# Performance work log

Hardware: AMD Instinct MI355X
Metric: run time of the kernel (lower is better)

## Reference

```python
import jax, jax.numpy as jnp
import numpy as np

B = 1024          # sub (= obj) batch size
NUME = 20000      # num entities
NUMR = 8          # num relations
NET = 2 * NUMR + 1  # hetero edge types: r, -r, self
DIMT = 28         # time encoding dim
DIME = 100        # entity embedding dim
DIM = 200         # emb module output dim
H = 4             # history length
HEADS = 4         # GAT heads
OH = DIM // HEADS # GAT per-head out dim
N0 = 160000       # layer-0 src nodes
N1 = 40000        # layer-0 dst / layer-1 src nodes
R = 2 * B * H     # unique roots = layer-1 dst nodes
E0 = 60000        # edges per etype, layer 0
E1 = 16000        # edges per etype, layer 1
K = 500000        # copy mask entries
DIMR = 100        # relation embedding dim
HATT = 4          # self-attention heads
OA = DIM // HATT  # per-head q/k/v dim (Attention out_dim//h)
DIN0 = DIME + DIMT
DIN1 = DIM + DIMT


def setup_inputs() -> dict:
    key = jax.random.key(0)
    ks = jax.random.split(key, 48)
    ri = jax.random.randint
    nrm = lambda i, shp, s=0.05: jax.random.normal(ks[i], shp, jnp.float32) * s
    d = {}
    d['sub'] = ri(ks[0], (B,), 0, NUME)
    d['obj'] = ri(ks[1], (B,), 0, NUME)
    d['rel'] = ri(ks[2], (B,), 0, NUMR)
    d['ts'] = 1000
    d['nid0'] = ri(ks[3], (N0,), 0, NUME * 1000)
    d['root_idx'] = ri(ks[4], (2 * B * H,), 0, R)
    d['src0'] = ri(ks[5], (NET, E0), 0, N0)
    d['dst0'] = ri(ks[6], (NET, E0), 0, N1)
    d['src1'] = ri(ks[7], (NET, E1), 0, N1)
    d['dst1'] = ri(ks[8], (NET, E1), 0, R)
    d['copy_rows'] = ri(ks[9], (K,), 0, 2 * B)
    d['copy_cols'] = ri(ks[10], (K,), 0, NUME)
    # parameters
    d['emb_table'] = nrm(11, (NUME, DIME))
    d['time_freq'] = jnp.asarray(1.0 / 10 ** np.linspace(0, 9, DIMT), jnp.float32)
    d['time_phase'] = jnp.zeros((DIMT,), jnp.float32)
    d['Wg0'] = nrm(12, (NET, DIN0, HEADS, OH))
    d['al0'] = nrm(13, (NET, HEADS, OH))
    d['ar0'] = nrm(14, (NET, HEADS, OH))
    d['bg0'] = jnp.zeros((NET, DIM), jnp.float32)
    d['Wg1'] = nrm(15, (NET, DIN1, HEADS, OH))
    d['al1'] = nrm(16, (NET, HEADS, OH))
    d['ar1'] = nrm(17, (NET, HEADS, OH))
    d['bg1'] = jnp.zeros((NET, DIM), jnp.float32)
    d['ln0_w'] = jnp.ones((H * DIM,), jnp.float32)
    d['ln0_b'] = jnp.zeros((H * DIM,), jnp.float32)
    d['Wq'] = nrm(18, (HATT, DIM, OA))
    d['bq'] = jnp.zeros((HATT, OA), jnp.float32)
    d['Wv'] = nrm(19, (HATT, DIM, OA))
    d['bv'] = jnp.zeros((HATT, OA), jnp.float32)
    d['ln1_w'] = jnp.ones((H * DIM,), jnp.float32)
    d['ln1_b'] = jnp.zeros((H * DIM,), jnp.float32)
    d['Wd1'] = nrm(20, (H * DIM, DIM))
    d['bd1'] = jnp.zeros((DIM,), jnp.float32)
    d['srel_emb'] = nrm(21, (NUMR, DIMR))
    d['orel_emb'] = nrm(22, (NUMR, DIMR))
    d['Wsub'] = nrm(23, (DIM + DIMR, NUME))
    d['bsub'] = jnp.zeros((NUME,), jnp.float32)
    d['Wobj'] = nrm(24, (DIM + DIMR, NUME))
    d['bobj'] = jnp.zeros((NUME,), jnp.float32)
    d['csrel_emb'] = nrm(25, (NUMR, DIMR))
    d['corel_emb'] = nrm(26, (NUMR, DIMR))
    d['cWsub'] = nrm(27, (DIM + DIMR, NUME))
    d['cbsub'] = jnp.zeros((NUME,), jnp.float32)
    d['cWobj'] = nrm(28, (DIM + DIMR, NUME))
    d['cbobj'] = jnp.zeros((NUME,), jnp.float32)
    return d


def _temb(nid, ts, tf, tp):
    t = (ts - nid // NUME).astype(jnp.float32)
    return jnp.cos(t[:, None] * tf + tp)


def _gat(x, Wg, al, ar, bg, src, dst, nd):
    # heterogeneous GATConv over NET relation types, mean-aggregated (DGL HeteroGraphConv)
    msg = jnp.zeros((nd, HEADS, OH), x.dtype)
    for r in range(NET):
        s, d = src[r], dst[r]
        fs = jnp.einsum('ei,iho->eho', x[s], Wg[r])                     # [E,h,o] src feats per edge
        er_n = (jnp.einsum('ni,iho->nho', x[:nd], Wg[r]) * ar[r]).sum(-1)  # [nd,h]
        el = (fs * al[r]).sum(-1)                                       # [E,h]
        e = jax.nn.leaky_relu(el + er_n[d], 0.2)
        m = jax.ops.segment_max(e, d, num_segments=nd)
        a = jnp.exp(e - m[d])
        z = jax.ops.segment_sum(a, d, num_segments=nd)
        alpha = a / z[d]
        msg = msg + jax.ops.segment_sum(alpha[:, :, None] * fs, d, num_segments=nd)
    return jax.nn.relu((msg.reshape(nd, HEADS * OH) + bg.sum(0)) / NET)


def _ln(x, w, b):
    mu = x.mean(-1, keepdims=True)
    v = ((x - mu) ** 2).mean(-1, keepdims=True)
    return (x - mu) / jnp.sqrt(v + 1e-5) * w + b


def reference(sub, obj, rel, ts, nid0, root_idx, src0, dst0, src1, dst1, copy_rows, copy_cols, emb_table, time_freq, time_phase, Wg0, al0, ar0, bg0, Wg1, al1, ar1, bg1, ln0_w, ln0_b, Wq, bq, Wv, bv, ln1_w, ln1_b, Wd1, bd1, srel_emb, orel_emb, Wsub, bsub, Wobj, bobj, csrel_emb, corel_emb, cWsub, cbsub, cWobj, cbobj):
    # --- EmbModule: entity emb + time enc + 2-layer hetero GAT over sampled blocks ---
    h = emb_table[nid0 % NUME]                                   # [N0, DIME]
    x = jnp.concatenate([h, _temb(nid0, ts, time_freq, time_phase)], 1)
    h = _gat(x, Wg0, al0, ar0, bg0, src0, dst0, N1)              # [N1, DIM]
    x = jnp.concatenate([h, _temb(nid0[:N1], ts, time_freq, time_phase)], 1)
    h = _gat(x, Wg1, al1, ar1, bg1, src1, dst1, R)               # [R, DIM]
    hid = h[root_idx].reshape(2 * B, H * DIM)                    # [2B, H*DIM]
    # --- Copy mechanism (on detached last-history embedding) ---
    ch = jax.lax.stop_gradient(hid[:, -DIM:])
    raw_sub = jnp.concatenate([ch[B:], corel_emb[rel]], 1) @ cWsub + cbsub
    raw_obj = jnp.concatenate([ch[:B], csrel_emb[rel]], 1) @ cWobj + cbobj
    raw = jnp.concatenate([raw_sub, raw_obj], 0)                 # [2B, NUME]
    masked = jnp.full((2 * B, NUME), -100.0, raw.dtype).at[copy_rows, copy_cols].set(raw[copy_rows, copy_cols])
    csub, cobj = masked[:B], masked[B:]
    # --- Gen layers: LN -> SelfAttention -> LN -> dense ---
    x = _ln(hid, ln0_w, ln0_b)
    xs = x.reshape(2 * B, H, DIM)
    q = jnp.einsum('bse,heo->bhso', xs, Wq) + bq[:, None, :]     # k == q (w_q reused in source)
    att = jax.nn.softmax(jnp.einsum('bhso,bhto->bhst', q, q), axis=2)  # torch softmax(dim=1)
    v = jnp.einsum('bse,heo->bhso', xs, Wv) + bv[:, None, :]
    ans = jnp.einsum('bhst,bhto->bhso', att, v)                  # [2B,h,S,OA]
    x = jax.nn.relu(ans.transpose(0, 2, 1, 3).reshape(2 * B, H * DIM))
    x = _ln(x, ln1_w, ln1_b)
    x = jax.nn.relu(x @ Wd1 + bd1)                               # [2B, DIM]
    sub_emb, obj_emb = x[:B], x[B:]
    sub_pred = jnp.concatenate([obj_emb, orel_emb[rel]], 1) @ Wsub + bsub
    obj_pred = jnp.concatenate([sub_emb, srel_emb[rel]], 1) @ Wobj + bobj
    return (sub_pred, obj_pred, csub, cobj)
```

## Files before the change

kernel.cpp:

```cpp
#include <hip/hip_runtime.h>
#include <hip/hip_bf16.h>
#include <math.h>

typedef __hip_bfloat16 bf16;
typedef __attribute__((ext_vector_type(8))) short short8;
typedef __attribute__((ext_vector_type(4))) float f32x4;

#define BQ 1024
#define NUME 20000
#define NET 17
#define DIMT 28
#define DIME 100
#define DIM 200
#define HEADS 4
#define OH 50
#define N0 160000
#define N1 40000
#define RNODES 8192
#define E0 60000
#define E1 16000
#define KK 500000
#define DIMR 100
#define HATT 4
#define OA 50
#define DIN0 128
#define DIN1 228
#define HD 800
#define NROWS 2048
#define PKS 10
#define PNT 1250
#define TABW 136

__device__ __forceinline__ float b2f(bf16 v){ return __bfloat162float(v); }
__device__ __forceinline__ bf16 f2b(float v){ return __float2bfloat16(v); }
__device__ __forceinline__ float bs2f(unsigned short u){ return __uint_as_float((unsigned)u << 16); }
__device__ __forceinline__ unsigned short f2bu(float v){ bf16 t = f2b(v); return *reinterpret_cast<unsigned short*>(&t); }

static constexpr int CVT_NREG = 29;
static constexpr int CVT_N[CVT_NREG] = {
  2000000, 28, 28, 435200, 3400, 3400, 3400, 775200, 3400, 3400, 3400,
  800, 800, 40000, 200, 40000, 200, 800, 800, 160000, 200, 800, 800,
  20000, 20000, 800, 800, 20000, 20000
};
static constexpr int CVT_DIN[CVT_NREG] = {
  12,13,14,15,16,17,18,19,20,21,22,23,24,25,26,27,28,29,30,31,32,33,34,36,38,39,40,42,44
};
struct CvtSrcs { const void* p[CVT_NREG]; };
struct CvtMeta { int cum[CVT_NREG+1]; int bcum[CVT_NREG+1]; };

__global__ __launch_bounds__(64) void k_detect(const unsigned* tfw, unsigned* flag){
  if (threadIdx.x == 0) flag[0] = ((tfw[0] & 0xFFFFu) == 0u) ? 1u : 0u;
}

__global__ __launch_bounds__(256) void k_cvt(CvtSrcs srcs, CvtMeta meta, bf16* dst, const unsigned* flagp){
  int b = blockIdx.x;
  int r = 0;
  while (meta.bcum[r+1] <= b) r++;
  int i = (b - meta.bcum[r])*256 + threadIdx.x;
  int n = meta.cum[r+1] - meta.cum[r];
  if (i >= n) return;
  bool f32m = flagp[0] != 0u;
  bf16 v;
  if (f32m) v = f2b(((const float*)srcs.p[r])[i]);
  else      v = ((const bf16*)srcs.p[r])[i];
  dst[meta.cum[r] + i] = v;
}

__global__ __launch_bounds__(256) void k_fill_u32(unsigned* p, unsigned v, long n){
  long i = (long)blockIdx.x*256 + threadIdx.x;
  if (i < n) p[i] = v;
}

__global__ __launch_bounds__(256) void k_fill_out(void* outb, const unsigned* flagp){
  bool f32m = flagp[0] != 0u;
  long nwords = f32m ? (long)2*BQ*NUME : (long)BQ*NUME;
  long i = (long)blockIdx.x*256 + threadIdx.x;
  if (i >= nwords) return;
  unsigned* p = (unsigned*)((char*)outb + (size_t)2*BQ*NUME * (f32m ? 4 : 2));
  p[i] = f32m ? 0xC2C80000u : 0xC2C8C2C8u;
}

__global__ __launch_bounds__(256) void k_prep_w(const bf16* Wg, const bf16* al, const bf16* ar,
                                                float* wal, float* war, int DIN){
  int idx = blockIdx.x*256 + threadIdx.x;
  int total = NET*DIN*4;
  if (idx >= total) return;
  int h = idx & 3; int ri = idx >> 2; int i = ri % DIN; int r = ri / DIN;
  const bf16* wrow = Wg + ((size_t)(r*DIN + i))*HEADS*OH + h*OH;
  const bf16* alr = al + (size_t)(r*HEADS + h)*OH;
  const bf16* arr = ar + (size_t)(r*HEADS + h)*OH;
  float sl=0.f, sr=0.f;
  for (int o=0;o<OH;o++){ float w=b2f(wrow[o]); sl += w*b2f(alr[o]); sr += w*b2f(arr[o]); }
  wal[idx]=sl; war[idx]=sr;
}

__global__ __launch_bounds__(256) void k_pack(const bf16* Wg, bf16* wpk, int DIN, int KS){
  int idx = blockIdx.x*256 + threadIdx.x;
  int total = NET*KS*13*512;
  if (idx >= total) return;
  int j = idx & 7, lane = (idx>>3) & 63;
  int rem = idx >> 9;
  int nt = rem % 13, rks = rem / 13;
  int ks = rks % KS, r = rks / KS;
  int k = ks*32 + (lane>>4)*8 + j;
  int n = nt*16 + (lane&15);
  bf16 v = f2b(0.f);
  if (k < DIN && n < 200) v = Wg[((size_t)r*DIN + k)*200 + n];
  wpk[idx] = v;
}

__global__ __launch_bounds__(256) void k_pack_walr(const float* wal, const float* war, bf16* wpkE,
                                                   int DIN, int KS){
  int idx = blockIdx.x*256 + threadIdx.x;
  int total = KS*9*512;
  if (idx >= total) return;
  int j = idx & 7, lane = (idx>>3) & 63;
  int rem = idx >> 9;
  int nt = rem % 9, ks = rem / 9;
  int k = ks*32 + (lane>>4)*8 + j;
  int c = nt*16 + (lane&15);
  float v = 0.f;
  if (k < DIN && c < TABW){
    int r = c >> 3, q = c & 7;
    const float* wsrc = (q < 4) ? wal : war;
    v = wsrc[((size_t)r*DIN + k)*4 + (q & 3)];
  }
  wpkE[idx] = f2b(v);
}

template<int DIN, int KS>
__global__ __launch_bounds__(256) void k_elr(const bf16* __restrict__ x, const bf16* __restrict__ wpkE,
                                             float* __restrict__ tab){
  constexpr int KM = KS*32;
  constexpr int SR = KM + 8;
  __shared__ bf16 xs[64*SR];
  int rb = blockIdx.x*64;
  int t = threadIdx.x;
  constexpr int CH = KM/4;
  for (int c = t; c < 64*CH; c += 256){
    int m = c / CH, j4 = c % CH;
    uint2 v = make_uint2(0u,0u);
    if (j4*4 < DIN) v = *(const uint2*)(x + (size_t)(rb+m)*DIN + j4*4);
    *(uint2*)(xs + m*SR + j4*4) = v;
  }
  __syncthreads();
  int lane = t & 63, w = t >> 6;
  int n_idx = lane & 15, quad = lane >> 4;
  const short8* wp8 = (const short8*)wpkE;
  for (int mt=0; mt<4; mt++){
    short8 a[KS];
    const bf16* ab = xs + (size_t)(mt*16 + n_idx)*SR + quad*8;
    #pragma unroll
    for (int ks=0; ks<KS; ks++) a[ks] = *(const short8*)(ab + ks*32);
    int m = rb + mt*16 + n_idx;
    for (int nt=w; nt<9; nt+=4){
      const short8* bp = wp8 + (size_t)nt*64 + lane;
      f32x4 acc = {0.f,0.f,0.f,0.f};
      #pragma unroll
      for (int ks=0; ks<KS; ks++){
        short8 b = bp[(size_t)ks*9*64];
        acc = __builtin_amdgcn_mfma_f32_16x16x32_bf16(b, a[ks], acc, 0, 0, 0);
      }
      int nbase = nt*16 + quad*4;
      if (nbase < TABW){
        float4 o; o.x=acc[0]; o.y=acc[1]; o.z=acc[2]; o.w=acc[3];
        *(float4*)(tab + (size_t)m*TABW + nbase) = o;
      }
    }
  }
}

__global__ __launch_bounds__(256) void k_edge_lite(const float* __restrict__ tab,
                                                   const int* __restrict__ src, const int* __restrict__ dst,
                                                   bf16* abuf, float* z, int nE, int nd){
  int idx = blockIdx.x*256 + threadIdx.x;
  if (idx >= NET*nE) return;
  int r = idx / nE;
  int s = src[idx], d = dst[idx];
  float4 el = *(const float4*)(tab + (size_t)s*TABW + r*8);
  float4 er = *(const float4*)(tab + (size_t)d*TABW + r*8 + 4);
  float ev[4] = {el.x+er.x, el.y+er.y, el.z+er.z, el.w+er.w};
  float* zp = z + ((size_t)r*nd + d)*4;
  bf16* ao = abuf + (size_t)idx*4;
  #pragma unroll
  for (int h=0;h<4;h++){
    float v = ev[h];
    v = v>0.f ? v : 0.2f*v;
    float a = expf(fminf(v, 80.f));
    ao[h] = f2b(a);
    atomicAdd(&zp[h], a);
  }
}

template<int DIN>
__global__ __launch_bounds__(256) void k_er(const bf16* __restrict__ x, const float* __restrict__ war,
                                            bf16* __restrict__ er, int nd){
  int idx = blockIdx.x*256 + threadIdx.x;
  if (idx >= NET*nd) return;
  int r = idx / nd, n = idx % nd;
  const ushort4* xr = (const ushort4*)(x + (size_t)n*DIN);
  const float4* w = (const float4*)(war + (size_t)r*DIN*4);
  float a0=0.f,a1=0.f,a2=0.f,a3=0.f;
  #pragma unroll 4
  for (int i=0;i<DIN/4;i++){
    ushort4 xv = xr[i];
    float x0=bs2f(xv.x), x1=bs2f(xv.y), x2=bs2f(xv.z), x3=bs2f(xv.w);
    float4 w0=w[4*i], w1=w[4*i+1], w2=w[4*i+2], w3=w[4*i+3];
    a0 += x0*w0.x + x1*w1.x + x2*w2.x + x3*w3.x;
    a1 += x0*w0.y + x1*w1.y + x2*w2.y + x3*w3.y;
    a2 += x0*w0.z + x1*w1.z + x2*w2.z + x3*w3.z;
    a3 += x0*w0.w + x1*w1.w + x2*w2.w + x3*w3.w;
  }
  bf16* e = er + (size_t)idx*4;
  e[0]=f2b(a0); e[1]=f2b(a1); e[2]=f2b(a2); e[3]=f2b(a3);
}

template<int DIN>
__global__ __launch_bounds__(256) void k_edge(const bf16* __restrict__ x, const float* __restrict__ wal,
                                              const bf16* __restrict__ er,
                                              const int* __restrict__ src, const int* __restrict__ dst,
                                              bf16* abuf, float* z, int nE, int nd){
  int idx = blockIdx.x*256 + threadIdx.x;
  if (idx >= NET*nE) return;
  int r = idx / nE;
  int s = src[idx], d = dst[idx];
  const ushort4* xr = (const ushort4*)(x + (size_t)s*DIN);
  const float4* w = (const float4*)(wal + (size_t)r*DIN*4);
  float a0=0.f,a1=0.f,a2=0.f,a3=0.f;
  #pragma unroll 4
  for (int i=0;i<DIN/4;i++){
    ushort4 xv = xr[i];
    float x0=bs2f(xv.x), x1=bs2f(xv.y), x2=bs2f(xv.z), x3=bs2f(xv.w);
    float4 w0=w[4*i], w1=w[4*i+1], w2=w[4*i+2], w3=w[4*i+3];
    a0 += x0*w0.x + x1*w1.x + x2*w2.x + x3*w3.x;
    a1 += x0*w0.y + x1*w1.y + x2*w2.y + x3*w3.y;
    a2 += x0*w0.z + x1*w1.z + x2*w2.z + x3*w3.z;
    a3 += x0*w0.w + x1*w1.w + x2*w2.w + x3*w3.w;
  }
  float acc[4] = {a0,a1,a2,a3};
  const bf16* ern = er + ((size_t)r*nd + d)*4;
  float* zp = z + ((size_t)r*nd + d)*4;
  bf16* ao = abuf + (size_t)idx*4;
  #pragma unroll
  for (int h=0;h<4;h++){
    float v = acc[h] + b2f(ern[h]);
    v = v>0.f ? v : 0.2f*v;
    float a = expf(fminf(v, 80.f));
    ao[h] = f2b(a);
    atomicAdd(&zp[h], a);
  }
}

__global__ __launch_bounds__(256) void k_count(const int* __restrict__ dst, long n, unsigned* cnt){
  long i = (long)blockIdx.x*256 + threadIdx.x;
  if (i >= n) return;
  atomicAdd(&cnt[dst[i]], 1u);
}

__global__ __launch_bounds__(256) void k_scan(const unsigned* __restrict__ cnt, unsigned* offs, unsigned* cur, int n){
  __shared__ unsigned part[256];
  __shared__ unsigned tot;
  int t = threadIdx.x;
  int chunk = (n + 255)/256;
  int lo = t*chunk, hi = lo+chunk; if (hi > n) hi = n; if (lo > n) lo = n;
  unsigned s = 0;
  for (int i=lo;i<hi;i++) s += cnt[i];
  part[t] = s;
  __syncthreads();
  if (t==0){
    unsigned r = 0;
    for (int i=0;i<256;i++){ unsigned v = part[i]; part[i] = r; r += v; }
    tot = r;
  }
  __syncthreads();
  unsigned run = part[t];
  for (int i=lo;i<hi;i++){ offs[i]=run; cur[i]=run; run += cnt[i]; }
  if (t==0) offs[n] = tot;
}

__global__ __launch_bounds__(256) void k_fillcsr(const int* __restrict__ dst, long n, unsigned* cur, int* posar){
  long i = (long)blockIdx.x*256 + threadIdx.x;
  if (i >= n) return;
  unsigned pos = atomicAdd(&cur[dst[i]], 1u);
  posar[i] = (int)pos;
}

template<int DIN, int KS>
__global__ __launch_bounds__(256) void k_acc_mfma(const bf16* __restrict__ x, const bf16* __restrict__ wpk,
                                                  const bf16* __restrict__ abuf, const float* __restrict__ z,
                                                  const int* __restrict__ src, const int* __restrict__ dst,
                                                  const int* __restrict__ posar,
                                                  float* msg, bf16* fbuf, int nE, int nd, int r0, int mode){
  constexpr int KM = KS*32;
  constexpr int SR = KM + 8;
  __shared__ bf16 xs[64*SR];
  __shared__ float alpha_s[64*4];
  __shared__ int sdst[64], ssrc[64], spos[64];
  int r = r0 + blockIdx.y;
  int eb = blockIdx.x*64;
  int me = min(64, nE - eb);
  int t = threadIdx.x;
  if (t < 64){
    int v_src=0, v_dst=0, v_pos=0;
    if (t < me){
      v_src = src[(size_t)r*nE + eb + t];
      v_dst = dst[(size_t)r*nE + eb + t];
      if (posar) v_pos = posar[(size_t)(r - r0)*nE + eb + t];
    }
    ssrc[t]=v_src; sdst[t]=v_dst; spos[t]=v_pos;
  }
  __syncthreads();
  {
    int m = t>>2, h = t&3;
    float al = 0.f;
    if (m < me){
      float a = b2f(abuf[((size_t)r*nE + eb + m)*4 + h]);
      float zz = z[((size_t)r*nd + sdst[m])*4 + h];
      al = a / fmaxf(zz, 1e-30f);
    }
    alpha_s[m*4+h] = al;
  }
  constexpr int CH = KM/4;
  for (int c = t; c < 64*CH; c += 256){
    int m = c / CH, j4 = c % CH;
    uint2 v = make_uint2(0u,0u);
    if (m < me && j4*4 < DIN) v = *(const uint2*)(x + (size_t)ssrc[m]*DIN + j4*4);
    *(uint2*)(xs + m*SR + j4*4) = v;
  }
  __syncthreads();

  int lane = t & 63, w = t >> 6;
  int n_idx = lane & 15, quad = lane >> 4;
  const short8* wpk8 = (const short8*)wpk;
  for (int mt=0; mt<4; mt++){
    short8 a[KS];
    const bf16* abase = xs + (size_t)(mt*16 + n_idx)*SR + quad*8;
    #pragma unroll
    for (int ks=0; ks<KS; ks++) a[ks] = *(const short8*)(abase + ks*32);
    int m = mt*16 + n_idx;
    for (int nt=w; nt<13; nt+=4){
      const short8* bp = wpk8 + (((size_t)r*KS)*13 + nt)*64 + lane;
      f32x4 acc = {0.f,0.f,0.f,0.f};
      #pragma unroll
      for (int ks=0; ks<KS; ks++){
        short8 b = bp[(size_t)ks*13*64];
        acc = __builtin_amdgcn_mfma_f32_16x16x32_bf16(b, a[ks], acc, 0, 0, 0);
      }
      int nbase = nt*16 + quad*4;
      if (nbase < 200 && m < me){
        if (mode == 0){
          #pragma unroll
          for (int reg=0; reg<4; reg++){
            int n = nbase + reg;
            atomicAdd(&msg[(size_t)sdst[m]*200 + n], acc[reg] * alpha_s[m*4 + n/50]);
          }
        } else {
          ushort4 pk;
          { int n=nbase;   pk.x = f2bu(acc[0] * alpha_s[m*4 + n/50]); }
          { int n=nbase+1; pk.y = f2bu(acc[1] * alpha_s[m*4 + n/50]); }
          { int n=nbase+2; pk.z = f2bu(acc[2] * alpha_s[m*4 + n/50]); }
          { int n=nbase+3; pk.w = f2bu(acc[3] * alpha_s[m*4 + n/50]); }
          *(ushort4*)(fbuf + (size_t)spos[m]*200 + nbase) = pk;
        }
      }
    }
  }
}

__global__ __launch_bounds__(256) void k_gather_seq(const bf16* __restrict__ F, const unsigned* __restrict__ offs,
                                                    float* __restrict__ msg, int nd, int accum){
  int w = threadIdx.x >> 6, lane = threadIdx.x & 63;
  int d = blockIdx.x*4 + w;
  if (d >= nd) return;
  unsigned k0 = offs[d], k1 = offs[d+1];
  if (lane < 50){
    float a0=0.f, a1=0.f, a2=0.f, a3=0.f;
    for (unsigned k=k0; k<k1; k++){
      ushort4 v = *(const ushort4*)(F + (size_t)k*200 + lane*4);
      a0 += bs2f(v.x); a1 += bs2f(v.y); a2 += bs2f(v.z); a3 += bs2f(v.w);
    }
    float4* out = (float4*)(msg + (size_t)d*200 + lane*4);
    if (accum){ float4 p = *out; a0 += p.x; a1 += p.y; a2 += p.z; a3 += p.w; }
    float4 o; o.x=a0; o.y=a1; o.z=a2; o.w=a3;
    *out = o;
  }
}

__global__ __launch_bounds__(256) void k_bgs(const bf16* bg0, const bf16* bg1, float* bgs0, float* bgs1){
  int j = blockIdx.x*256 + threadIdx.x;
  if (j < DIM){ float s=0.f; for(int r=0;r<NET;r++) s += b2f(bg0[r*DIM+j]); bgs0[j]=s; }
  else if (j < 2*DIM){ int jj=j-DIM; float s=0.f; for(int r=0;r<NET;r++) s += b2f(bg1[r*DIM+jj]); bgs1[jj]=s; }
}

__global__ __launch_bounds__(256) void k_build_x0(const int* nid0, const int* ts_p, const bf16* emb,
                                                  const bf16* tf, const bf16* tp, bf16* x0){
  long idx = (long)blockIdx.x*256 + threadIdx.x;
  if (idx >= (long)N0*DIN0) return;
  int n = idx / DIN0, j = idx % DIN0;
  int nid = nid0[n];
  bf16 v;
  if (j < DIME) v = emb[(size_t)(nid % NUME)*DIME + j];
  else {
    float t = (float)(ts_p[0] - nid / NUME);
    int jj = j - DIME;
    v = f2b(cosf(t * b2f(tf[jj]) + b2f(tp[jj])));
  }
  x0[idx] = v;
}

__global__ __launch_bounds__(256) void k_build_x1(const int* nid0, const int* ts_p, const float* msg0,
                                                  const float* bgs0, const bf16* tf, const bf16* tp, bf16* x1){
  long idx = (long)blockIdx.x*256 + threadIdx.x;
  if (idx >= (long)N1*DIN1) return;
  int n = idx / DIN1, j = idx % DIN1;
  bf16 v;
  if (j < DIM){
    v = f2b(fmaxf((msg0[(size_t)n*DIM + j] + bgs0[j]) * (1.0f/NET), 0.0f));
  } else {
    int nid = nid0[n];
    float t = (float)(ts_p[0] - nid / NUME);
    int jj = j - DIM;
    v = f2b(cosf(t * b2f(tf[jj]) + b2f(tp[jj])));
  }
  x1[idx] = v;
}

__global__ __launch_bounds__(256) void k_hid(const float* msg1, const float* bgs1, const int* root_idx, float* hid){
  long idx = (long)blockIdx.x*256 + threadIdx.x;
  if (idx >= (long)NROWS*HD) return;
  int b = idx / HD, c = idx % HD;
  int s = c / DIM, j = c % DIM;
  int n = root_idx[b*4 + s];
  hid[idx] = fmaxf((msg1[(size_t)n*DIM + j] + bgs1[j]) * (1.0f/NET), 0.0f);
}

__global__ __launch_bounds__(256) void k_att_ln(const float* __restrict__ hid,
                                                const bf16* ln0w, const bf16* ln0b,
                                                const bf16* Wq, const bf16* bq,
                                                const bf16* Wv, const bf16* bv,
                                                const bf16* ln1w, const bf16* ln1b,
                                                float* __restrict__ x3){
  __shared__ float xs[HD], qs[HD], vs[HD], att_s[64], red[16];
  __shared__ float mu_s, rs_s;
  int b = blockIdx.x, t = threadIdx.x;
  int lane = t & 63, wid = t >> 6;
  const float* xr = hid + (size_t)b*HD;
  float s=0.f, s2=0.f;
  for (int j=t;j<HD;j+=256){ float v=xr[j]; s+=v; s2+=v*v; }
  for (int off=32; off; off>>=1){ s += __shfl_down(s,off); s2 += __shfl_down(s2,off); }
  if (lane==0){ red[wid]=s; red[8+wid]=s2; }
  __syncthreads();
  if (t==0){
    float S = red[0]+red[1]+red[2]+red[3];
    float S2 = red[8]+red[9]+red[10]+red[11];
    float mu = S * (1.0f/HD);
    float var = fmaxf(S2 * (1.0f/HD) - mu*mu, 0.f);
    mu_s = mu; rs_s = rsqrtf(var + 1e-5f);
  }
  __syncthreads();
  { float mu=mu_s, rs=rs_s;
    for (int j=t;j<HD;j+=256) xs[j] = (xr[j]-mu)*rs*b2f(ln0w[j]) + b2f(ln0b[j]); }
  __syncthreads();
  for (int idx=t; idx<HD; idx+=256){
    int ha = idx/200, srow=(idx%200)/50, o=idx%50;
    const float* xrow = xs + srow*200;
    const bf16* wq = Wq + (size_t)ha*DIM*OA + o;
    const bf16* wv = Wv + (size_t)ha*DIM*OA + o;
    float q=0.f, v=0.f;
    for (int e=0;e<DIM;e++){ float xv=xrow[e]; q += xv*b2f(wq[(size_t)e*OA]); v += xv*b2f(wv[(size_t)e*OA]); }
    qs[idx] = q + b2f(bq[ha*OA+o]);
    vs[idx] = v + b2f(bv[ha*OA+o]);
  }
  __syncthreads();
  if (t < 64){
    int ha=t>>4, srow=(t>>2)&3, tt=t&3;
    const float* qa = qs + ha*200 + srow*50;
    const float* qb = qs + ha*200 + tt*50;
    float sc=0.f;
    for (int o=0;o<50;o++) sc += qa[o]*qb[o];
    att_s[ha*16 + srow*4 + tt] = sc;
  }
  __syncthreads();
  if (t < 16){
    int ha=t>>2, tt=t&3;
    float m=-1e30f;
    for (int srow=0;srow<4;srow++) m = fmaxf(m, att_s[ha*16+srow*4+tt]);
    float ex[4]; float zz=0.f;
    for (int srow=0;srow<4;srow++){ ex[srow]=expf(att_s[ha*16+srow*4+tt]-m); zz+=ex[srow]; }
    for (int srow=0;srow<4;srow++) att_s[ha*16+srow*4+tt] = ex[srow]/zz;
  }
  __syncthreads();
  for (int idx=t; idx<HD; idx+=256){
    int ha = idx/200, srow=(idx%200)/50, o=idx%50;
    float a=0.f;
    for (int tt=0;tt<4;tt++) a += att_s[ha*16+srow*4+tt]*vs[ha*200+tt*50+o];
    xs[srow*200 + ha*50 + o] = fmaxf(a, 0.f);
  }
  __syncthreads();
  s=0.f; s2=0.f;
  for (int j=t;j<HD;j+=256){ float v=xs[j]; s+=v; s2+=v*v; }
  for (int off=32; off; off>>=1){ s += __shfl_down(s,off); s2 += __shfl_down(s2,off); }
  if (lane==0){ red[wid]=s; red[8+wid]=s2; }
  __syncthreads();
  if (t==0){
    float S = red[0]+red[1]+red[2]+red[3];
    float S2 = red[8]+red[9]+red[10]+red[11];
    float mu = S * (1.0f/HD);
    float var = fmaxf(S2 * (1.0f/HD) - mu*mu, 0.f);
    mu_s = mu; rs_s = rsqrtf(var + 1e-5f);
  }
  __syncthreads();
  { float mu=mu_s, rs=rs_s;
    for (int j=t;j<HD;j+=256) x3[(size_t)b*HD + j] = (xs[j]-mu)*rs*b2f(ln1w[j]) + b2f(ln1b[j]); }
}

__global__ __launch_bounds__(256) void k_d1(const float* x3, const bf16* Wd1, const bf16* bd1, float* x4){
  __shared__ float xs[8*HD];
  int rb = blockIdx.x*8, t = threadIdx.x;
  for (int idx=t; idx<8*HD; idx+=256) xs[idx] = x3[(size_t)rb*HD + idx];
  __syncthreads();
  if (t < DIM){
    float acc[8] = {0,0,0,0,0,0,0,0};
    for (int k=0;k<HD;k++){
      float w = b2f(Wd1[(size_t)k*DIM + t]);
      #pragma unroll
      for (int r=0;r<8;r++) acc[r] += xs[r*HD+k]*w;
    }
    float bb = b2f(bd1[t]);
    for (int r=0;r<8;r++) x4[(size_t)(rb+r)*DIM + t] = fmaxf(acc[r]+bb, 0.f);
  }
}

__global__ __launch_bounds__(256) void k_pack_pred(const void* Wsub, const void* Wobj, bf16* wpkP,
                                                    const unsigned* flagp){
  long idx = (long)blockIdx.x*256 + threadIdx.x;
  long total = (long)2*PKS*PNT*512;
  if (idx >= total) return;
// ... 95 lines not shown
  int rb = blockIdx.y*16;
  int cb = blockIdx.x*512;
  int t = threadIdx.x;
  for (int idx=t; idx<16*300; idx+=256){
    int r = idx/300, i = idx%300;
    int row = rb + r;
    float v = (i < DIM) ? xemb[(size_t)row*DIM + i]
                        : b2f(relemb[(size_t)rel[row]*DIMR + (i-DIM)]);
    As[r*304+i] = v;
  }
  __syncthreads();
  int c0 = cb + t, c1 = cb + 256 + t;
  bool g0 = c0 < NUME, g1 = c1 < NUME;
  float acc0[16], acc1[16];
  #pragma unroll
  for (int r=0;r<16;r++){ acc0[r]=0.f; acc1[r]=0.f; }
  if (f32m){
    const float* W32 = (const float*)W;
    for (int k=0;k<300;k++){
      float w0 = g0 ? W32[(size_t)k*NUME + c0] : 0.f;
      float w1 = g1 ? W32[(size_t)k*NUME + c1] : 0.f;
      #pragma unroll
      for (int r=0;r<16;r++){ float a = As[r*304+k]; acc0[r] += a*w0; acc1[r] += a*w1; }
    }
  } else {
    const bf16* W16 = (const bf16*)W;
    for (int k=0;k<300;k++){
      float w0 = g0 ? b2f(W16[(size_t)k*NUME + c0]) : 0.f;
      float w1 = g1 ? b2f(W16[(size_t)k*NUME + c1]) : 0.f;
      #pragma unroll
      for (int r=0;r<16;r++){ float a = As[r*304+k]; acc0[r] += a*w0; acc1[r] += a*w1; }
    }
  }
  #pragma unroll
  for (int rr=0; rr<2; rr++){
    int c = rr ? c1 : c0;
    float* acc = rr ? acc1 : acc0;
    if (c < NUME){
      float bb = b2f(bias[c]);
      for (int r=0;r<16;r++){
        size_t oi = elem_off + (size_t)(rb+r)*NUME + c;
        float val = acc[r] + bb;
        if (f32m) ((float*)outb)[oi] = val; else ((bf16*)outb)[oi] = f2b(val);
      }
    }
  }
}

__global__ __launch_bounds__(256) void k_transpose(const void* in, bf16* out, int rows, int cols,
                                                   const unsigned* flagp){
  __shared__ bf16 tile[32][33];
  bool f32m = flagp[0] != 0u;
  int c0 = blockIdx.x*32, r0 = blockIdx.y*32;
  int tx = threadIdx.x % 32, ty = threadIdx.x / 32;
  for (int rr=ty; rr<32; rr+=8){
    int r = r0+rr, c = c0+tx;
    if (r<rows && c<cols){
      size_t i = (size_t)r*cols + c;
      tile[rr][tx] = f32m ? f2b(((const float*)in)[i]) : ((const bf16*)in)[i];
    }
  }
  __syncthreads();
  for (int rr=ty; rr<32; rr+=8){
    int ocol = c0+rr, orow = r0+tx;
    if (ocol<cols && orow<rows) out[(size_t)ocol*rows + orow] = tile[tx][rr];
  }
}

__global__ __launch_bounds__(256) void k_scatter(const int* copy_rows, const int* copy_cols, const int* rel,
                                                 const float* hid, const bf16* csrel, const bf16* corel,
                                                 const bf16* cWsubT, const bf16* cWobjT,
                                                 const bf16* cbsub, const bf16* cbobj,
                                                 void* outb, const unsigned* flagp){
  bool f32m = flagp[0] != 0u;
  int wid = threadIdx.x >> 6, lane = threadIdx.x & 63;
  long k = (long)blockIdx.x*4 + wid;
  if (k >= KK) return;
  int row = copy_rows[k], col = copy_cols[k];
  const float* chrow; const bf16* re; const bf16* wt; float bias_v;
  if (row < BQ){
    chrow = hid + ((size_t)(BQ+row))*HD + 600;
    re = corel + (size_t)rel[row]*DIMR;
    wt = cWsubT + (size_t)col*300;
    bias_v = b2f(cbsub[col]);
  } else {
    int rr = row - BQ;
    chrow = hid + ((size_t)rr)*HD + 600;
    re = csrel + (size_t)rel[rr]*DIMR;
    wt = cWobjT + (size_t)col*300;
    bias_v = b2f(cbobj[col]);
  }
  float s = 0.f;
  for (int i=lane; i<300; i+=64){
    float a = (i < DIM) ? chrow[i] : b2f(re[i-DIM]);
    s += a * b2f(wt[i]);
  }
  for (int off=32; off; off>>=1) s += __shfl_down(s, off);
  if (lane==0){
    size_t oi = (size_t)2*BQ*NUME + (size_t)row*NUME + col;
    float val = s + bias_v;
    if (f32m) ((float*)outb)[oi] = val; else ((bf16*)outb)[oi] = f2b(val);
  }
}

static inline dim3 GS(long n){ return dim3((unsigned)((n + 255)/256)); }

extern "C" void kernel_launch(void* const* d_in, const int* in_sizes, int n_in,
                              void* d_out, int out_size, void* d_ws, size_t ws_size,
                              hipStream_t stream){
  const int* rel       = (const int*)d_in[2];
  const int* ts_p      = (const int*)d_in[3];
  const int* nid0      = (const int*)d_in[4];
  const int* root_idx  = (const int*)d_in[5];
  const int* src0      = (const int*)d_in[6];
  const int* dst0      = (const int*)d_in[7];
  const int* src1      = (const int*)d_in[8];
  const int* dst1      = (const int*)d_in[9];
  const int* copy_rows = (const int*)d_in[10];
  const int* copy_cols = (const int*)d_in[11];
  const void* Wsub  = d_in[35];
  const void* Wobj  = d_in[37];
  const void* cWsub = d_in[41];
  const void* cWobj = d_in[43];

  char* base = (char*)d_ws;
  size_t off = 0;
  auto alloc = [&](size_t bytes)->char*{
    char* p = base + off; off = (off + bytes + 255) & ~(size_t)255; return p;
  };
  unsigned* flagp = (unsigned*)alloc(256);
  long cvt_total = 0; for (int i=0;i<CVT_NREG;i++) cvt_total += CVT_N[i];
  bf16* normb = (bf16*)alloc((size_t)cvt_total*2);
  bf16* x0    = (bf16*)alloc((size_t)N0*DIN0*2);
  bf16* x1    = (bf16*)alloc((size_t)N1*DIN1*2);
  float* msg0 = (float*)alloc((size_t)N1*DIM*4);
  float* wal0 = (float*)alloc((size_t)NET*DIN0*4*4);
  float* war0 = (float*)alloc((size_t)NET*DIN0*4*4);
  float* wal1 = (float*)alloc((size_t)NET*DIN1*4*4);
  float* war1 = (float*)alloc((size_t)NET*DIN1*4*4);
  float* bgs0 = (float*)alloc(DIM*4);
  float* bgs1 = (float*)alloc(DIM*4);
  bf16* wpk0  = (bf16*)alloc((size_t)NET*4*13*512*2);
  bf16* wpk1  = (bf16*)alloc((size_t)NET*8*13*512*2);
  bf16* wpkE0 = (bf16*)alloc((size_t)4*9*512*2);
  bf16* wpkE1 = (bf16*)alloc((size_t)8*9*512*2);
  size_t arena = off;
  char* P1 = base + arena;
  bf16*  a0b = (bf16*)P1;
  float* z0  = (float*)(P1 + (size_t)NET*E0*8);
  size_t ext1 = (size_t)NET*E0*8 + (size_t)NET*N1*16;
  char* A = base + arena;
  bf16*  a1b  = (bf16*)A;
  float* z1   = (float*)(A + (size_t)NET*E1*8);
  float* msg1 = (float*)(A + (size_t)NET*E1*8 + (size_t)NET*RNODES*16);
  size_t msg1_off = (size_t)NET*E1*8 + (size_t)NET*RNODES*16;
  float* hid  = (float*)(A + msg1_off + (size_t)RNODES*DIM*4);
  size_t hid_off = msg1_off + (size_t)RNODES*DIM*4;
  float* x3   = (float*)(A + hid_off + (size_t)NROWS*HD*4);
  size_t x3_off = hid_off + (size_t)NROWS*HD*4;
  float* x4   = (float*)(A + x3_off + (size_t)NROWS*HD*4);
  size_t ext2 = x3_off + (size_t)NROWS*HD*4 + (size_t)NROWS*DIM*4;
  bf16* cWsubT = (bf16*)x0;
  bf16* cWobjT = (bf16*)((char*)x0 + (size_t)NUME*300*2);

  size_t extmax = ext1 > ext2 ? ext1 : ext2;
  size_t tail = (arena + extmax + 255) & ~(size_t)255;
  size_t cntsz = (((size_t)(N1+1)*4) + 255) & ~(size_t)255;
  unsigned* cnt  = (unsigned*)(base + tail);
  unsigned* offs = (unsigned*)(base + tail + cntsz);
  unsigned* cur  = (unsigned*)(base + tail + 2*cntsz);
  size_t posar_sz = (((size_t)NET*E0*4) + 255) & ~(size_t)255;
  int* posar = (int*)(base + tail + 3*cntsz);
  size_t F_off = tail + 3*cntsz + posar_sz;
  bf16* fbuf = (bf16*)(base + F_off);
  size_t fcap = (ws_size > F_off) ? (ws_size - F_off) : 0;
  size_t relF0 = (size_t)E0*200*2, relF1 = (size_t)E1*200*2;
  int nrelc0 = (int)((fcap / relF0 < (size_t)NET) ? (fcap / relF0) : (size_t)NET);
  int nrelc1 = (int)((fcap / relF1 < (size_t)NET) ? (fcap / relF1) : (size_t)NET);
  float* tab0 = (float*)fbuf;
  float* tab1 = (float*)fbuf;
  bool elrok0 = fcap >= (size_t)N0*TABW*4;
  bool elrok1 = fcap >= (size_t)N1*TABW*4;
  bf16* er0f = (bf16*)x1;
  bf16* er1f = (bf16*)x0;
  size_t wpkP_sz = (size_t)2*PKS*PNT*512*2;
  size_t Apack_sz = (size_t)2*1024*320*2;
  bf16* wpkP  = (bf16*)(base + F_off);
  bf16* Apack = (bf16*)(base + F_off + wpkP_sz);
  bool predok = fcap >= (wpkP_sz + Apack_sz);

  long cum[CVT_NREG+1]; cum[0]=0;
  for (int i=0;i<CVT_NREG;i++) cum[i+1] = cum[i] + CVT_N[i];
  auto NP = [&](int i)->const bf16*{ return normb + cum[i]; };
  const bf16 *nEmb=NP(0), *nTf=NP(1), *nTp=NP(2), *nWg0=NP(3), *nAl0=NP(4), *nAr0=NP(5), *nBg0=NP(6),
             *nWg1=NP(7), *nAl1=NP(8), *nAr1=NP(9), *nBg1=NP(10), *nLn0w=NP(11), *nLn0b=NP(12),
             *nWq=NP(13), *nBq=NP(14), *nWv=NP(15), *nBv=NP(16), *nLn1w=NP(17), *nLn1b=NP(18),
             *nWd1=NP(19), *nBd1=NP(20), *nSrel=NP(21), *nOrel=NP(22), *nBsub=NP(23), *nBobj=NP(24),
             *nCsrel=NP(25), *nCorel=NP(26), *nCbsub=NP(27), *nCbobj=NP(28);

  k_detect<<<dim3(1),64,0,stream>>>((const unsigned*)d_in[13], flagp);
  CvtSrcs srcs;
  for (int i=0;i<CVT_NREG;i++) srcs.p[i] = d_in[CVT_DIN[i]];
  CvtMeta meta;
  { int c=0, bc=0;
    for (int i=0;i<CVT_NREG;i++){ meta.cum[i]=c; meta.bcum[i]=bc; c+=CVT_N[i]; bc += (CVT_N[i]+255)/256; }
    meta.cum[CVT_NREG]=c; meta.bcum[CVT_NREG]=bc;
    k_cvt<<<dim3((unsigned)bc),256,0,stream>>>(srcs, meta, normb, flagp);
  }
  k_fill_u32<<<GS((long)NET*N1*4),256,0,stream>>>((unsigned*)z0, 0u, (long)NET*N1*4);
  k_fill_out<<<GS((long)2*BQ*NUME),256,0,stream>>>(d_out, flagp);
  k_prep_w<<<GS(NET*DIN0*4),256,0,stream>>>(nWg0, nAl0, nAr0, wal0, war0, DIN0);
  k_prep_w<<<GS(NET*DIN1*4),256,0,stream>>>(nWg1, nAl1, nAr1, wal1, war1, DIN1);
  k_pack<<<GS((long)NET*4*13*512),256,0,stream>>>(nWg0, wpk0, DIN0, 4);
  k_pack<<<GS((long)NET*8*13*512),256,0,stream>>>(nWg1, wpk1, DIN1, 8);
  k_pack_walr<<<GS((long)4*9*512),256,0,stream>>>(wal0, war0, wpkE0, DIN0, 4);
  k_pack_walr<<<GS((long)8*9*512),256,0,stream>>>(wal1, war1, wpkE1, DIN1, 8);
  k_bgs<<<GS(2*DIM),256,0,stream>>>(nBg0, nBg1, bgs0, bgs1);
  k_build_x0<<<GS((long)N0*DIN0),256,0,stream>>>(nid0, ts_p, nEmb, nTf, nTp, x0);

  if (elrok0){
    k_elr<DIN0,4><<<dim3(N0/64),256,0,stream>>>(x0, wpkE0, tab0);
    k_edge_lite<<<GS((long)NET*E0),256,0,stream>>>(tab0, src0, dst0, a0b, z0, E0, N1);
  } else {
    k_er<DIN0><<<GS((long)NET*N1),256,0,stream>>>(x0, war0, er0f, N1);
    k_edge<DIN0><<<GS((long)NET*E0),256,0,stream>>>(x0, wal0, er0f, src0, dst0, a0b, z0, E0, N1);
  }
  if (nrelc0 >= 1){
    for (int r0=0; r0<NET; r0+=nrelc0){
      int nr = (NET - r0 < nrelc0) ? (NET - r0) : nrelc0;
      long nEd = (long)nr*E0;
      k_fill_u32<<<GS((long)N1+1),256,0,stream>>>(cnt, 0u, (long)N1+1);
      k_count<<<GS(nEd),256,0,stream>>>(dst0 + (size_t)r0*E0, nEd, cnt);
      k_scan<<<dim3(1),256,0,stream>>>(cnt, offs, cur, N1);
      k_fillcsr<<<GS(nEd),256,0,stream>>>(dst0 + (size_t)r0*E0, nEd, cur, posar);
      k_acc_mfma<DIN0,4><<<dim3((E0+63)/64, nr),256,0,stream>>>(x0, wpk0, a0b, z0, src0, dst0, posar,
                                                                 msg0, fbuf, E0, N1, r0, 1);
      k_gather_seq<<<dim3((N1+3)/4),256,0,stream>>>(fbuf, offs, msg0, N1, r0>0 ? 1 : 0);
    }
  } else {
    k_fill_u32<<<GS((long)N1*DIM),256,0,stream>>>((unsigned*)msg0, 0u, (long)N1*DIM);
    k_acc_mfma<DIN0,4><<<dim3((E0+63)/64, NET),256,0,stream>>>(x0, wpk0, a0b, z0, src0, dst0, (int*)nullptr,
                                                                msg0, (bf16*)nullptr, E0, N1, 0, 0);
  }

  k_build_x1<<<GS((long)N1*DIN1),256,0,stream>>>(nid0, ts_p, msg0, bgs0, nTf, nTp, x1);
  k_fill_u32<<<GS((long)NET*RNODES*4),256,0,stream>>>((unsigned*)z1, 0u, (long)NET*RNODES*4);
  if (elrok1){
    k_elr<DIN1,8><<<dim3(N1/64),256,0,stream>>>(x1, wpkE1, tab1);
    k_edge_lite<<<GS((long)NET*E1),256,0,stream>>>(tab1, src1, dst1, a1b, z1, E1, RNODES);
  } else {
    k_er<DIN1><<<GS((long)NET*RNODES),256,0,stream>>>(x1, war1, er1f, RNODES);
    k_edge<DIN1><<<GS((long)NET*E1),256,0,stream>>>(x1, wal1, er1f, src1, dst1, a1b, z1, E1, RNODES);
  }
  if (nrelc1 >= 1){
    for (int r0=0; r0<NET; r0+=nrelc1){
      int nr = (NET - r0 < nrelc1) ? (NET - r0) : nrelc1;
      long nEd = (long)nr*E1;
      k_fill_u32<<<GS((long)RNODES+1),256,0,stream>>>(cnt, 0u, (long)RNODES+1);
      k_count<<<GS(nEd),256,0,stream>>>(dst1 + (size_t)r0*E1, nEd, cnt);
      k_scan<<<dim3(1),256,0,stream>>>(cnt, offs, cur, RNODES);
      k_fillcsr<<<GS(nEd),256,0,stream>>>(dst1 + (size_t)r0*E1, nEd, cur, posar);
      k_acc_mfma<DIN1,8><<<dim3((E1+63)/64, nr),256,0,stream>>>(x1, wpk1, a1b, z1, src1, dst1, posar,
                                                                 msg1, fbuf, E1, RNODES, r0, 1);
      k_gather_seq<<<dim3((RNODES+3)/4),256,0,stream>>>(fbuf, offs, msg1, RNODES, r0>0 ? 1 : 0);
    }
  } else {
    k_fill_u32<<<GS((long)RNODES*DIM),256,0,stream>>>((unsigned*)msg1, 0u, (long)RNODES*DIM);
    k_acc_mfma<DIN1,8><<<dim3((E1+63)/64, NET),256,0,stream>>>(x1, wpk1, a1b, z1, src1, dst1, (int*)nullptr,
                                                                msg1, (bf16*)nullptr, E1, RNODES, 0, 0);
  }

  if (predok)
    k_pack_pred<<<GS((long)2*PKS*PNT*512),256,0,stream>>>(Wsub, Wobj, wpkP, flagp);

  k_hid<<<GS((long)NROWS*HD),256,0,stream>>>(msg1, bgs1, root_idx, hid);
  k_transpose<<<dim3(625,10),256,0,stream>>>(cWsub, cWsubT, 300, NUME, flagp);
  k_transpose<<<dim3(625,10),256,0,stream>>>(cWobj, cWobjT, 300, NUME, flagp);
  k_scatter<<<dim3((KK+3)/4),256,0,stream>>>(copy_rows, copy_cols, rel, hid, nCsrel, nCorel,
                                             cWsubT, cWobjT, nCbsub, nCbobj, d_out, flagp);

  k_att_ln<<<dim3(NROWS),256,0,stream>>>(hid, nLn0w, nLn0b, nWq, nBq, nWv, nBv, nLn1w, nLn1b, x3);
  k_d1<<<dim3(NROWS/8),256,0,stream>>>(x3, nWd1, nBd1, x4);

  if (predok){
    k_prep_pred<<<GS((long)2*1024*320),256,0,stream>>>(x4, nSrel, nOrel, rel, Apack);
    k_pred_mfma<<<dim3(79,16,2),256,0,stream>>>(Apack, wpkP, nBsub, nBobj, d_out, flagp);
  } else {
    k_pred<<<dim3(40,64),256,0,stream>>>(x4 + (size_t)BQ*DIM, nOrel, rel, Wsub, nBsub, d_out, 0, flagp);
    k_pred<<<dim3(40,64),256,0,stream>>>(x4,                  nSrel, rel, Wobj, nBobj, d_out, (size_t)BQ*NUME, flagp);
  }
  (void)in_sizes; (void)n_in; (void)out_size; (void)ws_size;
}
```

Before: 2.305 ms.

## Build per-relation CSR for all relations at once and process edges in sorted order

Result: no change. 2.279 ms (-1.1%).

```diff
diff --git a/kernel.cpp b/kernel.cpp
--- a/kernel.cpp
+++ b/kernel.cpp
@@ -30,6 +30,8 @@
 #define PKS 10
 #define PNT 1250
 #define TABW 136
+#define E0PAD 60032
+#define E1PAD 16000
 
 __device__ __forceinline__ float b2f(bf16 v){ return __bfloat162float(v); }
 __device__ __forceinline__ bf16 f2b(float v){ return __float2bfloat16(v); }
@@ -251,70 +253,74 @@
   }
 }
 
-__global__ __launch_bounds__(256) void k_count(const int* __restrict__ dst, long n, unsigned* cnt){
-  long i = (long)blockIdx.x*256 + threadIdx.x;
-  if (i >= n) return;
-  atomicAdd(&cnt[dst[i]], 1u);
-}
-
-__global__ __launch_bounds__(256) void k_scan(const unsigned* __restrict__ cnt, unsigned* offs, unsigned* cur, int n){
+__global__ __launch_bounds__(256) void k_count2(const int* __restrict__ dst, int nE, int nd, unsigned* cnt){
+  int i = blockIdx.x*256 + threadIdx.x;
+  if (i >= NET*nE) return;
+  int r = i / nE; int d = dst[i];
+  atomicAdd(&cnt[(size_t)r*nd + d], 1u);
+}
+
+__global__ __launch_bounds__(256) void k_scan2(const unsigned* __restrict__ cnt, unsigned* offs, unsigned* cur,
+                                               int nd, int nE, int nEpad){
   __shared__ unsigned part[256];
-  __shared__ unsigned tot;
-  int t = threadIdx.x;
-  int chunk = (n + 255)/256;
-  int lo = t*chunk, hi = lo+chunk; if (hi > n) hi = n; if (lo > n) lo = n;
+  int r = blockIdx.x, t = threadIdx.x;
+  unsigned base = (unsigned)(r*nEpad);
+  const unsigned* c = cnt + (size_t)r*nd;
+  unsigned* o  = offs + (size_t)r*(nd+1);
+  unsigned* cu = cur  + (size_t)r*(nd+1);
+  int chunk = (nd + 255)/256;
+  int lo = t*chunk, hi = lo+chunk; if (hi > nd) hi = nd; if (lo > nd) lo = nd;
   unsigned s = 0;
-  for (int i=lo;i<hi;i++) s += cnt[i];
+  for (int i=lo;i<hi;i++) s += c[i];
   part[t] = s;
   __syncthreads();
-  if (t==0){
-    unsigned r = 0;
-    for (int i=0;i<256;i++){ unsigned v = part[i]; part[i] = r; r += v; }
-    tot = r;
-  }
-  __syncthreads();
-  unsigned run = part[t];
-  for (int i=lo;i<hi;i++){ offs[i]=run; cur[i]=run; run += cnt[i]; }
-  if (t==0) offs[n] = tot;
-}
-
-__global__ __launch_bounds__(256) void k_fillcsr(const int* __restrict__ dst, long n, unsigned* cur, int* posar){
-  long i = (long)blockIdx.x*256 + threadIdx.x;
-  if (i >= n) return;
-  unsigned pos = atomicAdd(&cur[dst[i]], 1u);
-  posar[i] = (int)pos;
+  if (t==0){ unsigned run=0; for (int i=0;i<256;i++){ unsigned v=part[i]; part[i]=run; run+=v; } }
+  __syncthreads();
+  unsigned run = base + part[t];
+  for (int i=lo;i<hi;i++){ o[i]=run; cu[i]=run; run += c[i]; }
+  if (t==0) o[nd] = base + (unsigned)nE;
+}
+
+__global__ __launch_bounds__(256) void k_fillcsr2(const int* __restrict__ dst, int nE, int nd,
+                                                  unsigned* cur, int* ids){
+  int i = blockIdx.x*256 + threadIdx.x;
+  if (i >= NET*nE) return;
+  int r = i / nE, e = i - r*nE;
+  int d = dst[i];
+  unsigned pos = atomicAdd(&cur[(size_t)r*(nd+1) + d], 1u);
+  ids[pos] = e;
 }
 
 template<int DIN, int KS>
 __global__ __launch_bounds__(256) void k_acc_mfma(const bf16* __restrict__ x, const bf16* __restrict__ wpk,
                                                   const bf16* __restrict__ abuf, const float* __restrict__ z,
                                                   const int* __restrict__ src, const int* __restrict__ dst,
-                                                  const int* __restrict__ posar,
-                                                  float* msg, bf16* fbuf, int nE, int nd, int r0, int mode){
+                                                  const int* __restrict__ ids,
+                                                  float* msg, bf16* fbuf, int nE, int nEpad, int nd, int mode){
   constexpr int KM = KS*32;
   constexpr int SR = KM + 8;
   __shared__ bf16 xs[64*SR];
   __shared__ float alpha_s[64*4];
-  __shared__ int sdst[64], ssrc[64], spos[64];
-  int r = r0 + blockIdx.y;
-  int eb = blockIdx.x*64;
-  int me = min(64, nE - eb);
+  __shared__ int sdst[64], ssrc[64], sE[64];
+  int r = blockIdx.y;
+  int ls0 = blockIdx.x*64;
+  int me = min(64, nE - ls0);
   int t = threadIdx.x;
   if (t < 64){
-    int v_src=0, v_dst=0, v_pos=0;
+    int e = ls0 + t, vs=0, vd=0;
     if (t < me){
-      v_src = src[(size_t)r*nE + eb + t];
-      v_dst = dst[(size_t)r*nE + eb + t];
-      if (posar) v_pos = posar[(size_t)(r - r0)*nE + eb + t];
-    }
-    ssrc[t]=v_src; sdst[t]=v_dst; spos[t]=v_pos;
+      if (mode == 1) e = ids[(size_t)r*nEpad + ls0 + t];
+      vs = src[(size_t)r*nE + e];
+      vd = dst[(size_t)r*nE + e];
+    }
+    sE[t]=e; ssrc[t]=vs; sdst[t]=vd;
   }
   __syncthreads();
   {
     int m = t>>2, h = t&3;
     float al = 0.f;
     if (m < me){
-      float a = b2f(abuf[((size_t)r*nE + eb + m)*4 + h]);
+      float a = b2f(abuf[((size_t)r*nE + sE[m])*4 + h]);
       float zz = z[((size_t)r*nd + sdst[m])*4 + h];
       al = a / fmaxf(zz, 1e-30f);
     }
@@ -360,29 +366,30 @@
           { int n=nbase+1; pk.y = f2bu(acc[1] * alpha_s[m*4 + n/50]); }
           { int n=nbase+2; pk.z = f2bu(acc[2] * alpha_s[m*4 + n/50]); }
           { int n=nbase+3; pk.w = f2bu(acc[3] * alpha_s[m*4 + n/50]); }
-          *(ushort4*)(fbuf + (size_t)spos[m]*200 + nbase) = pk;
+          *(ushort4*)(fbuf + ((size_t)r*nEpad + ls0 + m)*200 + nbase) = pk;
         }
       }
     }
   }
 }
 
-__global__ __launch_bounds__(256) void k_gather_seq(const bf16* __restrict__ F, const unsigned* __restrict__ offs,
-                                                    float* __restrict__ msg, int nd, int accum){
+__global__ __launch_bounds__(256) void k_gather2(const bf16* __restrict__ F, const unsigned* __restrict__ offs,
+                                                 float* __restrict__ msg, int nd){
   int w = threadIdx.x >> 6, lane = threadIdx.x & 63;
   int d = blockIdx.x*4 + w;
   if (d >= nd) return;
-  unsigned k0 = offs[d], k1 = offs[d+1];
   if (lane < 50){
     float a0=0.f, a1=0.f, a2=0.f, a3=0.f;
-    for (unsigned k=k0; k<k1; k++){
-      ushort4 v = *(const ushort4*)(F + (size_t)k*200 + lane*4);
-      a0 += bs2f(v.x); a1 += bs2f(v.y); a2 += bs2f(v.z); a3 += bs2f(v.w);
-    }
-    float4* out = (float4*)(msg + (size_t)d*200 + lane*4);
-    if (accum){ float4 p = *out; a0 += p.x; a1 += p.y; a2 += p.z; a3 += p.w; }
+    for (int r=0; r<NET; r++){
+      unsigned k0 = offs[(size_t)r*(nd+1) + d];
+      unsigned k1 = offs[(size_t)r*(nd+1) + d + 1];
+      for (unsigned k=k0; k<k1; k++){
+        ushort4 v = *(const ushort4*)(F + (size_t)k*200 + lane*4);
+        a0 += bs2f(v.x); a1 += bs2f(v.y); a2 += bs2f(v.z); a3 += bs2f(v.w);
+      }
+    }
     float4 o; o.x=a0; o.y=a1; o.z=a2; o.w=a3;
-    *out = o;
+    *(float4*)(msg + (size_t)d*200 + lane*4) = o;
   }
 }
 
@@ -784,12 +791,12 @@
   char* A = base + arena;
   bf16*  a1b  = (bf16*)A;
   float* z1   = (float*)(A + (size_t)NET*E1*8);
-  float* msg1 = (float*)(A + (size_t)NET*E1*8 + (size_t)NET*RNODES*16);
   size_t msg1_off = (size_t)NET*E1*8 + (size_t)NET*RNODES*16;
-  float* hid  = (float*)(A + msg1_off + (size_t)RNODES*DIM*4);
+  float* msg1 = (float*)(A + msg1_off);
   size_t hid_off = msg1_off + (size_t)RNODES*DIM*4;
-  float* x3   = (float*)(A + hid_off + (size_t)NROWS*HD*4);
+  float* hid  = (float*)(A + hid_off);
   size_t x3_off = hid_off + (size_t)NROWS*HD*4;
+  float* x3   = (float*)(A + x3_off);
   float* x4   = (float*)(A + x3_off + (size_t)NROWS*HD*4);
   size_t ext2 = x3_off + (size_t)NROWS*HD*4 + (size_t)NROWS*DIM*4;
   bf16* cWsubT = (bf16*)x0;
@@ -797,18 +804,18 @@
 
   size_t extmax = ext1 > ext2 ? ext1 : ext2;
   size_t tail = (arena + extmax + 255) & ~(size_t)255;
-  size_t cntsz = (((size_t)(N1+1)*4) + 255) & ~(size_t)255;
+  size_t cnt_sz  = (((size_t)NET*N1*4) + 255) & ~(size_t)255;
+  size_t offs_sz = (((size_t)NET*(N1+1)*4) + 255) & ~(size_t)255;
+  size_t ids_sz  = (((size_t)NET*E0PAD*4) + 255) & ~(size_t)255;
   unsigned* cnt  = (unsigned*)(base + tail);
-  unsigned* offs = (unsigned*)(base + tail + cntsz);
-  unsigned* cur  = (unsigned*)(base + tail + 2*cntsz);
-  size_t posar_sz = (((size_t)NET*E0*4) + 255) & ~(size_t)255;
-  int* posar = (int*)(base + tail + 3*cntsz);
-  size_t F_off = tail + 3*cntsz + posar_sz;
+  unsigned* offs = (unsigned*)(base + tail + cnt_sz);
+  unsigned* cur  = (unsigned*)(base + tail + cnt_sz + offs_sz);
+  int* ids = (int*)(base + tail + cnt_sz + 2*offs_sz);
+  size_t F_off = tail + cnt_sz + 2*offs_sz + ids_sz;
   bf16* fbuf = (bf16*)(base + F_off);
   size_t fcap = (ws_size > F_off) ? (ws_size - F_off) : 0;
-  size_t relF0 = (size_t)E0*200*2, relF1 = (size_t)E1*200*2;
-  int nrelc0 = (int)((fcap / relF0 < (size_t)NET) ? (fcap / relF0) : (size_t)NET);
-  int nrelc1 = (int)((fcap / relF1 < (size_t)NET) ? (fcap / relF1) : (size_t)NET);
+  bool sortok0 = fcap >= (size_t)NET*E0PAD*400;
+  bool sortok1 = fcap >= (size_t)NET*E1PAD*400;
   float* tab0 = (float*)fbuf;
   float* tab1 = (float*)fbuf;
   bool elrok0 = fcap >= (size_t)N0*TABW*4;
@@ -857,22 +864,18 @@
     k_er<DIN0><<<GS((long)NET*N1),256,0,stream>>>(x0, war0, er0f, N1);
     k_edge<DIN0><<<GS((long)NET*E0),256,0,stream>>>(x0, wal0, er0f, src0, dst0, a0b, z0, E0, N1);
   }
-  if (nrelc0 >= 1){
-    for (int r0=0; r0<NET; r0+=nrelc0){
-      int nr = (NET - r0 < nrelc0) ? (NET - r0) : nrelc0;
-      long nEd = (long)nr*E0;
-      k_fill_u32<<<GS((long)N1+1),256,0,stream>>>(cnt, 0u, (long)N1+1);
-      k_count<<<GS(nEd),256,0,stream>>>(dst0 + (size_t)r0*E0, nEd, cnt);
-      k_scan<<<dim3(1),256,0,stream>>>(cnt, offs, cur, N1);
-      k_fillcsr<<<GS(nEd),256,0,stream>>>(dst0 + (size_t)r0*E0, nEd, cur, posar);
-      k_acc_mfma<DIN0,4><<<dim3((E0+63)/64, nr),256,0,stream>>>(x0, wpk0, a0b, z0, src0, dst0, posar,
-                                                                 msg0, fbuf, E0, N1, r0, 1);
-      k_gather_seq<<<dim3((N1+3)/4),256,0,stream>>>(fbuf, offs, msg0, N1, r0>0 ? 1 : 0);
-    }
+  if (sortok0){
+    k_fill_u32<<<GS((long)NET*N1),256,0,stream>>>(cnt, 0u, (long)NET*N1);
+    k_count2<<<GS((long)NET*E0),256,0,stream>>>(dst0, E0, N1, cnt);
+    k_scan2<<<dim3(NET),256,0,stream>>>(cnt, offs, cur, N1, E0, E0PAD);
+    k_fillcsr2<<<GS((long)NET*E0),256,0,stream>>>(dst0, E0, N1, cur, ids);
+    k_acc_mfma<DIN0,4><<<dim3((E0+63)/64, NET),256,0,stream>>>(x0, wpk0, a0b, z0, src0, dst0, ids,
+                                                                msg0, fbuf, E0, E0PAD, N1, 1);
+    k_gather2<<<dim3((N1+3)/4),256,0,stream>>>(fbuf, offs, msg0, N1);
   } else {
     k_fill_u32<<<GS((long)N1*DIM),256,0,stream>>>((unsigned*)msg0, 0u, (long)N1*DIM);
     k_acc_mfma<DIN0,4><<<dim3((E0+63)/64, NET),256,0,stream>>>(x0, wpk0, a0b, z0, src0, dst0, (int*)nullptr,
-                                                                msg0, (bf16*)nullptr, E0, N1, 0, 0);
+                                                                msg0, (bf16*)nullptr, E0, E0, N1, 0);
   }
 
   k_build_x1<<<GS((long)N1*DIN1),256,0,stream>>>(nid0, ts_p, msg0, bgs0, nTf, nTp, x1);
@@ -884,22 +887,18 @@
     k_er<DIN1><<<GS((long)NET*RNODES),256,0,stream>>>(x1, war1, er1f, RNODES);
     k_edge<DIN1><<<GS((long)NET*E1),256,0,stream>>>(x1, wal1, er1f, src1, dst1, a1b, z1, E1, RNODES);
   }
-  if (nrelc1 >= 1){
-    for (int r0=0; r0<NET; r0+=nrelc1){
-      int nr = (NET - r0 < nrelc1) ? (NET - r0) : nrelc1;
-      long nEd = (long)nr*E1;
-      k_fill_u32<<<GS((long)RNODES+1),256,0,stream>>>(cnt, 0u, (long)RNODES+1);
-      k_count<<<GS(nEd),256,0,stream>>>(dst1 + (size_t)r0*E1, nEd, cnt);
-      k_scan<<<dim3(1),256,0,stream>>>(cnt, offs, cur, RNODES);
-      k_fillcsr<<<GS(nEd),256,0,stream>>>(dst1 + (size_t)r0*E1, nEd, cur, posar);
-      k_acc_mfma<DIN1,8><<<dim3((E1+63)/64, nr),256,0,stream>>>(x1, wpk1, a1b, z1, src1, dst1, posar,
-                                                                 msg1, fbuf, E1, RNODES, r0, 1);
-      k_gather_seq<<<dim3((RNODES+3)/4),256,0,stream>>>(fbuf, offs, msg1, RNODES, r0>0 ? 1 : 0);
-    }
+  if (sortok1){
+    k_fill_u32<<<GS((long)NET*RNODES),256,0,stream>>>(cnt, 0u, (long)NET*RNODES);
+    k_count2<<<GS((long)NET*E1),256,0,stream>>>(dst1, E1, RNODES, cnt);
+    k_scan2<<<dim3(NET),256,0,stream>>>(cnt, offs, cur, RNODES, E1, E1PAD);
+    k_fillcsr2<<<GS((long)NET*E1),256,0,stream>>>(dst1, E1, RNODES, cur, ids);
+    k_acc_mfma<DIN1,8><<<dim3((E1+63)/64, NET),256,0,stream>>>(x1, wpk1, a1b, z1, src1, dst1, ids,
+                                                                msg1, fbuf, E1, E1PAD, RNODES, 1);
+    k_gather2<<<dim3((RNODES+3)/4),256,0,stream>>>(fbuf, offs, msg1, RNODES);
   } else {
     k_fill_u32<<<GS((long)RNODES*DIM),256,0,stream>>>((unsigned*)msg1, 0u, (long)RNODES*DIM);
     k_acc_mfma<DIN1,8><<<dim3((E1+63)/64, NET),256,0,stream>>>(x1, wpk1, a1b, z1, src1, dst1, (int*)nullptr,
-                                                                msg1, (bf16*)nullptr, E1, RNODES, 0, 0);
+                                                                msg1, (bf16*)nullptr, E1, E1, RNODES, 0);
   }
 
   if (predok)
```
